# Performance work log

Measured on AMD Instinct MI355X. Metric: run time of the kernel, lower is better.

## Reference

```python
import jax, jax.numpy as jnp
import numpy as np

NUM_HEADS = 12
D_MODEL = 768
D_HEAD = D_MODEL // NUM_HEADS


def setup_inputs() -> dict:
    key = jax.random.key(0)
    k_x, k_wqkv, k_bqkv, k_wo, k_bo = jax.random.split(key, 5)
    B, S = 1, 4096
    x = jax.random.normal(k_x, (B, S, D_MODEL), dtype=jnp.float32)
    # flax Dense default init: lecun_normal for kernel, zeros for bias
    w_qkv = jax.random.normal(k_wqkv, (D_MODEL, 3 * D_MODEL), dtype=jnp.float32) / np.sqrt(D_MODEL)
    b_qkv = jnp.zeros((3 * D_MODEL,), dtype=jnp.float32)
    w_o = jax.random.normal(k_wo, (D_MODEL, D_MODEL), dtype=jnp.float32) / np.sqrt(D_MODEL)
    b_o = jnp.zeros((D_MODEL,), dtype=jnp.float32)
    return {"x": x, "w_qkv": w_qkv, "b_qkv": b_qkv, "w_o": w_o, "b_o": b_o}


def reference(x, w_qkv, b_qkv, w_o, b_o):
    B, S, _ = x.shape
    H, Dh = NUM_HEADS, D_HEAD
    qkv = jnp.einsum('bsd,de->bse', x, w_qkv) + b_qkv  # [B,S,3*D]
    q, k, v = jnp.split(qkv, 3, axis=-1)
    # [B,S,D] -> [B,H,S,Dh]
    q = q.reshape(B, S, H, Dh).transpose(0, 2, 1, 3)
    k = k.reshape(B, S, H, Dh).transpose(0, 2, 1, 3)
    v = v.reshape(B, S, H, Dh).transpose(0, 2, 1, 3)
    logits = jnp.einsum('bhqd,bhkd->bhqk', q, k) / jnp.sqrt(jnp.float32(Dh))
    weights = jax.nn.softmax(logits, axis=-1)  # deterministic=True -> no dropout
    attn = jnp.einsum('bhqk,bhkd->bhqd', weights, v)
    attn = attn.transpose(0, 2, 1, 3).reshape(B, S, H * Dh)
    return jnp.einsum('bsd,de->bse', attn, w_o) + b_o
```

## Files before the change

### kernel.cpp

```cpp
#include <hip/hip_runtime.h>

typedef unsigned short u16;
typedef __attribute__((ext_vector_type(8))) short bf16x8;
typedef __attribute__((ext_vector_type(4))) float f32x4;

#define CST 0.18033688011112042f

#if __has_builtin(__builtin_amdgcn_exp2f)
#define EXP2(x) __builtin_amdgcn_exp2f(x)
#else
#define EXP2(x) exp2f(x)
#endif

__device__ inline u16 f2bf(float f) {
    unsigned u;
    __builtin_memcpy(&u, &f, 4);
    unsigned r = (u + 0x7FFF + ((u >> 16) & 1)) >> 16;
    return (u16)r;
}
__device__ inline unsigned pack2(float lo, float hi) {
    return (unsigned)f2bf(lo) | ((unsigned)f2bf(hi) << 16);
}
__device__ inline unsigned fbits(float f) {
    unsigned u;
    __builtin_memcpy(&u, &f, 4);
    return u;
}
__device__ inline f32x4 fzero() {
    f32x4 z = {0.f, 0.f, 0.f, 0.f};
    return z;
}
__device__ inline f32x4 mfma16(bf16x8 a, bf16x8 b, f32x4 c) {
    return __builtin_amdgcn_mfma_f32_16x16x32_bf16(a, b, c, 0, 0, 0);
}

__device__ inline void gld_lds16(const u16* g, u16* l) {
    __builtin_amdgcn_global_load_lds(
        reinterpret_cast<const __attribute__((address_space(1))) unsigned int*>(
            reinterpret_cast<uintptr_t>(g)),
        reinterpret_cast<__attribute__((address_space(3))) unsigned int*>(
            static_cast<unsigned int>(reinterpret_cast<uintptr_t>(l))),
        16, 0, 0);
}

#define NB_WQKV (72 * 24)
#define NB_WO   (24 * 24)
#define NB_CVT  (4096 * 768 / 2048)

__global__ __launch_bounds__(256) void prep(const float* __restrict__ x,
                                            const float* __restrict__ w_qkv,
                                            const float* __restrict__ w_o,
                                            u16* __restrict__ xb,
                                            u16* __restrict__ wqkvT,
                                            u16* __restrict__ woT) {
    __shared__ float tile[32][33];
    int bid = blockIdx.x;
    int t = threadIdx.x;
    if (bid < NB_WQKV + NB_WO) {
        const float* in;
        u16* out;
        int bx, by, R, C;
        if (bid < NB_WQKV) {
            in = w_qkv; out = wqkvT; R = 768; C = 2304;
            bx = bid % 72; by = bid / 72;
        } else {
            int b2 = bid - NB_WQKV;
            in = w_o; out = woT; R = 768; C = 768;
            bx = b2 % 24; by = b2 / 24;
        }
        int c0 = bx * 32, r0 = by * 32;
        int tx = t & 31, ty = t >> 5;
#pragma unroll
        for (int j = 0; j < 32; j += 8)
            tile[ty + j][tx] = in[(size_t)(r0 + ty + j) * C + c0 + tx];
        __syncthreads();
#pragma unroll
        for (int j = 0; j < 32; j += 8)
            out[(size_t)(c0 + ty + j) * R + r0 + tx] = f2bf(tile[tx][ty + j]);
    } else {
        int i = (bid - NB_WQKV - NB_WO) * 2048 + t * 8;
        float4 a = *(const float4*)(x + i);
        float4 b = *(const float4*)(x + i + 4);
        uint4 w;
        w.x = pack2(a.x, a.y);
        w.y = pack2(a.z, a.w);
        w.z = pack2(b.x, b.y);
        w.w = pack2(b.z, b.w);
        *(uint4*)(xb + i) = w;
    }
}

__global__ __launch_bounds__(256) void vtrans(const u16* __restrict__ qkv,
                                              u16* __restrict__ vt) {
    __shared__ u16 T[64 * 136];
    int t = threadIdx.x;
    int h = blockIdx.y, kv0 = blockIdx.x * 128;
    {
        int key = t >> 1, ch = (t & 1) * 32;
        const u16* vp = qkv + (size_t)(kv0 + key) * 2304 + 1536 + h * 64 + ch;
        u16 tmp[32];
        *(uint4*)&tmp[0]  = *(const uint4*)vp;
        *(uint4*)&tmp[8]  = *(const uint4*)(vp + 8);
        *(uint4*)&tmp[16] = *(const uint4*)(vp + 16);
        *(uint4*)&tmp[24] = *(const uint4*)(vp + 24);
        int k5 = key & 31, grp = key >> 5;
        int kp = (grp << 5) | (((k5 >> 2) & 3) << 3) | ((k5 >> 4) << 2) | (k5 & 3);
#pragma unroll
        for (int j = 0; j < 32; j++) T[(ch + j) * 136 + kp] = tmp[j];
    }
    __syncthreads();
    {
        int dh = t >> 2, kc = (t & 3) * 32;
        uint4 o0 = *(const uint4*)&T[dh * 136 + kc];
        uint4 o1 = *(const uint4*)&T[dh * 136 + kc + 8];
        uint4 o2 = *(const uint4*)&T[dh * 136 + kc + 16];
        uint4 o3 = *(const uint4*)&T[dh * 136 + kc + 24];
        u16* op = vt + ((size_t)(h * 64 + dh)) * 4096 + kv0 + kc;
        *(uint4*)op = o0;
        *(uint4*)(op + 8) = o1;
        *(uint4*)(op + 16) = o2;
        *(uint4*)(op + 24) = o3;
    }
}

template <int MT, bool OUT_F32, bool SCALE_Q>
__global__ __launch_bounds__(256) void gemm_bt(const u16* __restrict__ A,
                                               const u16* __restrict__ Bt,
                                               const float* __restrict__ bias,
                                               void* __restrict__ Cv,
                                               int M, int N, int K) {
    constexpr int MI = MT / 32;
    constexpr int NA = MT / 64;
    constexpr int AH = MT * 32;
    constexpr int BH = 128 * 32;
    __shared__ u16 As[2 * AH];
    __shared__ u16 Bs[2 * BH];

    int t = threadIdx.x;
    int wave = t >> 6, lane = t & 63, quad = lane >> 4, l16 = lane & 15;

    int gx = gridDim.x;
    int flat = blockIdx.y * gx + blockIdx.x;
    int cpx = (gx * gridDim.y) >> 3;
    int swz = (flat & 7) * cpx + (flat >> 3);
    int bx = swz % gx, by = swz / gx;

    int mbase = by * MT, nbase = bx * 128;
    int mw = (wave & 1) * (MT / 2), nw = (wave >> 1) * 64;

    f32x4 acc[MI][4];
#pragma unroll
    for (int i = 0; i < MI; i++)
#pragma unroll
        for (int j = 0; j < 4; j++) acc[i][j] = fzero();

    int xqs = (lane & 3) ^ ((lane >> 3) & 3);
    const u16* AgL[NA];
    u16* AsL[NA];
#pragma unroll
    for (int j = 0; j < NA; j++) {
        int rl = wave * (MT / 4) + j * 16 + (lane >> 2);
        AgL[j] = A + (size_t)(mbase + rl) * K + xqs * 8;
        AsL[j] = As + wave * (MT / 4) * 32 + j * 512;
    }
    const u16* BgL[2];
    u16* BsL[2];
#pragma unroll
    for (int j = 0; j < 2; j++) {
        int rl = wave * 32 + j * 16 + (lane >> 2);
        BgL[j] = Bt + (size_t)(nbase + rl) * K + xqs * 8;
        BsL[j] = Bs + wave * 1024 + j * 512;
    }

    auto STAGE = [&](int buf, int kt) {
#pragma unroll
        for (int j = 0; j < NA; j++) gld_lds16(AgL[j] + kt, AsL[j] + buf * AH);
#pragma unroll
        for (int j = 0; j < 2; j++) gld_lds16(BgL[j] + kt, BsL[j] + buf * BH);
    };

    int xq = quad ^ ((l16 >> 1) & 3);
    int afo[MI], bfo[4];
#pragma unroll
    for (int i = 0; i < MI; i++) afo[i] = (mw + i * 16 + l16) * 32 + xq * 8;
#pragma unroll
    for (int i = 0; i < 4; i++) bfo[i] = (nw + i * 16 + l16) * 32 + xq * 8;

    STAGE(0, 0);
    __syncthreads();

    int cur = 0;
    for (int kt = 0; kt < K; kt += 32) {
        if (kt + 32 < K) STAGE(cur ^ 1, kt + 32);

        const u16* AsB = As + cur * AH;
        const u16* BsB = Bs + cur * BH;
        bf16x8 af[MI], bfr[4];
#pragma unroll
        for (int i = 0; i < MI; i++) af[i] = *(const bf16x8*)&AsB[afo[i]];
#pragma unroll
        for (int i = 0; i < 4; i++) bfr[i] = *(const bf16x8*)&BsB[bfo[i]];
#pragma unroll
        for (int mi = 0; mi < MI; mi++)
#pragma unroll
            for (int ni = 0; ni < 4; ni++)
                acc[mi][ni] = mfma16(af[mi], bfr[ni], acc[mi][ni]);

        __syncthreads();
        cur ^= 1;
    }

#pragma unroll
    for (int ni = 0; ni < 4; ni++) {
        int col = nbase + nw + ni * 16 + l16;
        float bv = bias[col];
        float scale = (SCALE_Q && col < 768) ? CST : 1.0f;
#pragma unroll
        for (int mi = 0; mi < MI; mi++) {
#pragma unroll
            for (int r = 0; r < 4; r++) {
                int row = mbase + mw + mi * 16 + quad * 4 + r;
                float v = (acc[mi][ni][r] + bv) * scale;
                if (OUT_F32)
                    ((float*)Cv)[(size_t)row * N + col] = v;
                else
                    ((u16*)Cv)[(size_t)row * N + col] = f2bf(v);
            }
        }
    }
}

#define SEQ 4096
#define QKV_LD 2304

__global__ __launch_bounds__(256, 4) void attn_flash(const u16* __restrict__ qkv,
                                                     const u16* __restrict__ vt,
                                                     u16* __restrict__ attn) {
    __shared__ __align__(16) char smem[32768];

    int t = threadIdx.x;
    int wave = t >> 6, lane = t & 63, quad = lane >> 4, l16 = lane & 15;
    int kw = wave & 1, qw = wave >> 1;

    int flat = blockIdx.y * 64 + blockIdx.x;
    int swz = (flat & 7) * 96 + (flat >> 3);
    int h = swz >> 6;
    int q0 = (swz & 63) * 64;
    const int QOFF = h * 64, KOFF = 768 + h * 64;

    bf16x8 qf[2][2];
#pragma unroll
    for (int qs = 0; qs < 2; qs++) {
        const u16* qp = qkv + (size_t)(q0 + qw * 32 + qs * 16 + l16) * QKV_LD + QOFF + quad * 8;
        qf[qs][0] = *(const bf16x8*)(qp);
        qf[qs][1] = *(const bf16x8*)(qp + 32);
    }

    f32x4 o[2][4];
    f32x4 lacc[2];
#pragma unroll
    for (int qs = 0; qs < 2; qs++) {
        lacc[qs] = fzero();
#pragma unroll
        for (int j = 0; j < 4; j++) o[qs][j] = fzero();
    }
    bf16x8 vones;
#pragma unroll
    for (int j = 0; j < 8; j++) vones[j] = (short)0x3F80;

    const u16* kgl[2];
    const u16* vgl[2];
    int sofs[2];
#pragma unroll
    for (int j = 0; j < 2; j++) {
        int r = wave * 16 + j * 8 + (lane >> 3);
        int cd = (lane & 7) ^ ((lane >> 3) & 7);
        kgl[j] = qkv + (size_t)r * QKV_LD + KOFF + cd * 8;
        vgl[j] = vt + (size_t)(h * 64 + r) * SEQ + cd * 8;
        sofs[j] = (wave * 16 + j * 8) * 64;
    }

    auto STAGE = [&](int buf, int kv) {
        u16* kb = (u16*)(smem + buf * 8192);
        u16* vb = (u16*)(smem + 16384 + buf * 8192);
#pragma unroll
        for (int j = 0; j < 2; j++) gld_lds16(kgl[j] + (size_t)kv * QKV_LD, kb + sofs[j]);
#pragma unroll
        for (int j = 0; j < 2; j++) gld_lds16(vgl[j] + kv, vb + sofs[j]);
    };

    STAGE(0, 0);
    __syncthreads();

    int cur = 0;
    int x7 = l16 & 7;
    for (int kv0 = 0; kv0 < SEQ; kv0 += 64) {
        if (kv0 + 64 < SEQ) STAGE(cur ^ 1, kv0 + 64);

        const u16* KsB = (const u16*)(smem + cur * 8192);
        const u16* VsB = (const u16*)(smem + 16384 + cur * 8192);

        bf16x8 kf[2][2];
#pragma unroll
        for (int st = 0; st < 2; st++) {
            int r = kw * 32 + st * 16 + l16;
            kf[st][0] = *(const bf16x8*)&KsB[r * 64 + (quad ^ x7) * 8];
            kf[st][1] = *(const bf16x8*)&KsB[r * 64 + ((quad + 4) ^ x7) * 8];
        }
        bf16x8 vf[4];
#pragma unroll
        for (int nt = 0; nt < 4; nt++) {
            int r = nt * 16 + l16;
            vf[nt] = *(const bf16x8*)&VsB[r * 64 + ((kw * 4 + quad) ^ x7) * 8];
        }

        __builtin_amdgcn_s_setprio(1);
#pragma unroll
        for (int qs = 0; qs < 2; qs++) {
            f32x4 s0 = mfma16(kf[0][0], qf[qs][0], fzero());
            s0 = mfma16(kf[0][1], qf[qs][1], s0);
            f32x4 s1 = mfma16(kf[1][0], qf[qs][0], fzero());
            s1 = mfma16(kf[1][1], qf[qs][1], s1);
            float p00 = EXP2(s0[0]), p01 = EXP2(s0[1]);
            float p02 = EXP2(s0[2]), p03 = EXP2(s0[3]);
            float p10 = EXP2(s1[0]), p11 = EXP2(s1[1]);
            float p12 = EXP2(s1[2]), p13 = EXP2(s1[3]);
            uint4 pk;
            pk.x = __builtin_amdgcn_perm(fbits(p01), fbits(p00), 0x07060302u);
            pk.y = __builtin_amdgcn_perm(fbits(p03), fbits(p02), 0x07060302u);
            pk.z = __builtin_amdgcn_perm(fbits(p11), fbits(p10), 0x07060302u);
            pk.w = __builtin_amdgcn_perm(fbits(p13), fbits(p12), 0x07060302u);
            bf16x8 pf;
            __builtin_memcpy(&pf, &pk, 16);
            lacc[qs] = mfma16(pf, vones, lacc[qs]);
#pragma unroll
            for (int nt = 0; nt < 4; nt++)
                o[qs][nt] = mfma16(pf, vf[nt], o[qs][nt]);
        }
        __builtin_amdgcn_s_setprio(0);

        __syncthreads();
        cur ^= 1;
    }

    float* M0 = (float*)smem;
    float* Lm = (float*)(smem + 17408);
    if (l16 == 0) {
#pragma unroll
        for (int qs = 0; qs < 2; qs++)
#pragma unroll
            for (int r = 0; r < 4; r++)
                Lm[kw * 64 + qw * 32 + qs * 16 + quad * 4 + r] = lacc[qs][r];
    }
    if (kw == 1) {
#pragma unroll
        for (int nt = 0; nt < 4; nt++)
#pragma unroll
            for (int r = 0; r < 4; r++)
                M0[(qw * 32 + quad * 4 + r) * 68 + nt * 16 + l16] = o[0][nt][r];
    } else {
#pragma unroll
        for (int nt = 0; nt < 4; nt++)
#pragma unroll
            for (int r = 0; r < 4; r++)
                M0[(qw * 32 + 16 + quad * 4 + r) * 68 + nt * 16 + l16] = o[1][nt][r];
    }
    __syncthreads();
    if (kw == 0) {
#pragma unroll
        for (int r = 0; r < 4; r++) {
            int rw = qw * 32 + quad * 4 + r;
            float ltot = Lm[rw] + Lm[64 + rw];
            float inv = 1.0f / ltot;
            u16* op = attn + (size_t)(q0 + rw) * 768 + h * 64;
#pragma unroll
            for (int nt = 0; nt < 4; nt++) {
                float v = o[0][nt][r] + M0[rw * 68 + nt * 16 + l16];
                op[nt * 16 + l16] = f2bf(v * inv);
            }
        }
    } else {
#pragma unroll
        for (int r = 0; r < 4; r++) {
            int rw = qw * 32 + 16 + quad * 4 + r;
            float ltot = Lm[rw] + Lm[64 + rw];
            float inv = 1.0f / ltot;
            u16* op = attn + (size_t)(q0 + rw) * 768 + h * 64;
#pragma unroll
            for (int nt = 0; nt < 4; nt++) {
                float v = o[1][nt][r] + M0[rw * 68 + nt * 16 + l16];
                op[nt * 16 + l16] = f2bf(v * inv);
            }
        }
    }
}

extern "C" void kernel_launch(void* const* d_in, const int* in_sizes, int n_in,
                              void* d_out, int out_size, void* d_ws, size_t ws_size,
                              hipStream_t stream) {
    const float* x      = (const float*)d_in[0];
    const float* w_qkv  = (const float*)d_in[1];
    const float* b_qkv  = (const float*)d_in[2];
    const float* w_o    = (const float*)d_in[3];
    const float* b_o    = (const float*)d_in[4];
    float* out = (float*)d_out;

    u16* wqkvT = (u16*)d_ws;
    u16* woT   = wqkvT + (size_t)2304 * 768;
    u16* qkv   = woT + (size_t)768 * 768;
    u16* attnb = qkv + (size_t)4096 * 2304;
    u16* Vt    = attnb + (size_t)4096 * 768;
    u16* xb    = attnb;

    prep<<<dim3(NB_WQKV + NB_WO + NB_CVT), 256, 0, stream>>>(
        x, w_qkv, w_o, xb, wqkvT, woT);

    gemm_bt<128, false, true><<<dim3(2304 / 128, 4096 / 128), 256, 0, stream>>>(
        xb, wqkvT, b_qkv, qkv, 4096, 2304, 768);

    vtrans<<<dim3(SEQ / 128, 12), 256, 0, stream>>>(qkv, Vt);

    attn_flash<<<dim3(SEQ / 64, 12), 256, 0, stream>>>(qkv, Vt, attnb);

    gemm_bt<64, true, false><<<dim3(768 / 128, 4096 / 64), 256, 0, stream>>>(
        attnb, woT, b_o, out, 4096, 768, 768);
}
```

Measured before the change: 177.7 us.

## Fuse V transpose into QKV GEMM epilogue and shrink output-projection N tile

Removes the separate vtrans kernel. The QKV GEMM blocks that cover the V columns now write their bias-added tile transposed through shared memory straight into the Vt buffer, in the permuted key order attention expects. The V block of qkv is no longer written and read back. The GEMM template also gains an NT parameter, and the output projection now uses 64x64 tiles, doubling its grid to give more blocks for occupancy. The cost is extra syncs and an LDS staging pass in the V blocks, plus smaller tiles in the last GEMM, which lowers per-block data reuse.

```diff
diff --git a/kernel.cpp b/kernel.cpp
--- a/kernel.cpp
+++ b/kernel.cpp
@@ -5,6 +5,8 @@
 typedef __attribute__((ext_vector_type(4))) float f32x4;
 
 #define CST 0.18033688011112042f
+#define SEQ 4096
+#define QKV_LD 2304
 
 #if __has_builtin(__builtin_amdgcn_exp2f)
 #define EXP2(x) __builtin_amdgcn_exp2f(x)
@@ -90,51 +92,22 @@
     }
 }
 
-__global__ __launch_bounds__(256) void vtrans(const u16* __restrict__ qkv,
-                                              u16* __restrict__ vt) {
-    __shared__ u16 T[64 * 136];
-    int t = threadIdx.x;
-    int h = blockIdx.y, kv0 = blockIdx.x * 128;
-    {
-        int key = t >> 1, ch = (t & 1) * 32;
-        const u16* vp = qkv + (size_t)(kv0 + key) * 2304 + 1536 + h * 64 + ch;
-        u16 tmp[32];
-        *(uint4*)&tmp[0]  = *(const uint4*)vp;
-        *(uint4*)&tmp[8]  = *(const uint4*)(vp + 8);
-        *(uint4*)&tmp[16] = *(const uint4*)(vp + 16);
-        *(uint4*)&tmp[24] = *(const uint4*)(vp + 24);
-        int k5 = key & 31, grp = key >> 5;
-        int kp = (grp << 5) | (((k5 >> 2) & 3) << 3) | ((k5 >> 4) << 2) | (k5 & 3);
-#pragma unroll
-        for (int j = 0; j < 32; j++) T[(ch + j) * 136 + kp] = tmp[j];
-    }
-    __syncthreads();
-    {
-        int dh = t >> 2, kc = (t & 3) * 32;
-        uint4 o0 = *(const uint4*)&T[dh * 136 + kc];
-        uint4 o1 = *(const uint4*)&T[dh * 136 + kc + 8];
-        uint4 o2 = *(const uint4*)&T[dh * 136 + kc + 16];
-        uint4 o3 = *(const uint4*)&T[dh * 136 + kc + 24];
-        u16* op = vt + ((size_t)(h * 64 + dh)) * 4096 + kv0 + kc;
-        *(uint4*)op = o0;
-        *(uint4*)(op + 8) = o1;
-        *(uint4*)(op + 16) = o2;
-        *(uint4*)(op + 24) = o3;
-    }
-}
-
-template <int MT, bool OUT_F32, bool SCALE_Q>
+template <int MT, int NT, bool OUT_F32, bool SCALE_Q, bool FUSE_VT>
 __global__ __launch_bounds__(256) void gemm_bt(const u16* __restrict__ A,
                                                const u16* __restrict__ Bt,
                                                const float* __restrict__ bias,
                                                void* __restrict__ Cv,
+                                               u16* __restrict__ vt,
                                                int M, int N, int K) {
     constexpr int MI = MT / 32;
+    constexpr int NI = NT / 32;
     constexpr int NA = MT / 64;
+    constexpr int NB = NT / 64;
     constexpr int AH = MT * 32;
-    constexpr int BH = 128 * 32;
-    __shared__ u16 As[2 * AH];
-    __shared__ u16 Bs[2 * BH];
+    constexpr int BH = NT * 32;
+    __shared__ u16 pool[2 * AH + 2 * BH];
+    u16* As = pool;
+    u16* Bs = pool + 2 * AH;
 
     int t = threadIdx.x;
     int wave = t >> 6, lane = t & 63, quad = lane >> 4, l16 = lane & 15;
@@ -145,14 +118,14 @@
     int swz = (flat & 7) * cpx + (flat >> 3);
     int bx = swz % gx, by = swz / gx;
 
-    int mbase = by * MT, nbase = bx * 128;
-    int mw = (wave & 1) * (MT / 2), nw = (wave >> 1) * 64;
-
-    f32x4 acc[MI][4];
+    int mbase = by * MT, nbase = bx * NT;
+    int mw = (wave & 1) * (MT / 2), nw = (wave >> 1) * (NT / 2);
+
+    f32x4 acc[MI][NI];
 #pragma unroll
     for (int i = 0; i < MI; i++)
 #pragma unroll
-        for (int j = 0; j < 4; j++) acc[i][j] = fzero();
+        for (int j = 0; j < NI; j++) acc[i][j] = fzero();
 
     int xqs = (lane & 3) ^ ((lane >> 3) & 3);
     const u16* AgL[NA];
@@ -163,28 +136,28 @@
         AgL[j] = A + (size_t)(mbase + rl) * K + xqs * 8;
         AsL[j] = As + wave * (MT / 4) * 32 + j * 512;
     }
-    const u16* BgL[2];
-    u16* BsL[2];
-#pragma unroll
-    for (int j = 0; j < 2; j++) {
-        int rl = wave * 32 + j * 16 + (lane >> 2);
+    const u16* BgL[NB];
+    u16* BsL[NB];
+#pragma unroll
+    for (int j = 0; j < NB; j++) {
+        int rl = wave * (NT / 4) + j * 16 + (lane >> 2);
         BgL[j] = Bt + (size_t)(nbase + rl) * K + xqs * 8;
-        BsL[j] = Bs + wave * 1024 + j * 512;
+        BsL[j] = Bs + wave * (NT / 4) * 32 + j * 512;
     }
 
     auto STAGE = [&](int buf, int kt) {
 #pragma unroll
         for (int j = 0; j < NA; j++) gld_lds16(AgL[j] + kt, AsL[j] + buf * AH);
 #pragma unroll
-        for (int j = 0; j < 2; j++) gld_lds16(BgL[j] + kt, BsL[j] + buf * BH);
+        for (int j = 0; j < NB; j++) gld_lds16(BgL[j] + kt, BsL[j] + buf * BH);
     };
 
     int xq = quad ^ ((l16 >> 1) & 3);
-    int afo[MI], bfo[4];
+    int afo[MI], bfo[NI];
 #pragma unroll
     for (int i = 0; i < MI; i++) afo[i] = (mw + i * 16 + l16) * 32 + xq * 8;
 #pragma unroll
-    for (int i = 0; i < 4; i++) bfo[i] = (nw + i * 16 + l16) * 32 + xq * 8;
+    for (int i = 0; i < NI; i++) bfo[i] = (nw + i * 16 + l16) * 32 + xq * 8;
 
     STAGE(0, 0);
     __syncthreads();
@@ -195,23 +168,65 @@
 
         const u16* AsB = As + cur * AH;
         const u16* BsB = Bs + cur * BH;
-        bf16x8 af[MI], bfr[4];
+        bf16x8 af[MI], bfr[NI];
 #pragma unroll
         for (int i = 0; i < MI; i++) af[i] = *(const bf16x8*)&AsB[afo[i]];
 #pragma unroll
-        for (int i = 0; i < 4; i++) bfr[i] = *(const bf16x8*)&BsB[bfo[i]];
+        for (int i = 0; i < NI; i++) bfr[i] = *(const bf16x8*)&BsB[bfo[i]];
 #pragma unroll
         for (int mi = 0; mi < MI; mi++)
 #pragma unroll
-            for (int ni = 0; ni < 4; ni++)
+            for (int ni = 0; ni < NI; ni++)
                 acc[mi][ni] = mfma16(af[mi], bfr[ni], acc[mi][ni]);
 
         __syncthreads();
         cur ^= 1;
     }
 
-#pragma unroll
-    for (int ni = 0; ni < 4; ni++) {
+    if (FUSE_VT && nbase >= 1536) {
+        u16* T = pool;
+        int h0 = (nbase - 1536) >> 6;
+#pragma unroll
+        for (int pp = 0; pp < 2; pp++) {
+            if ((wave & 1) == pp) {
+#pragma unroll
+                for (int ni = 0; ni < NI; ni++) {
+                    int col = nw + ni * 16 + l16;
+                    float bv = bias[nbase + col];
+#pragma unroll
+                    for (int mi = 0; mi < MI; mi++) {
+#pragma unroll
+                        for (int r = 0; r < 4; r++) {
+                            int rowl = mi * 16 + quad * 4 + r;
+                            int k5 = rowl & 31, grp = rowl >> 5;
+                            int kp = (grp << 5) | (((k5 >> 2) & 3) << 3) |
+                                     ((k5 >> 4) << 2) | (k5 & 3);
+                            T[col * 72 + kp] = f2bf(acc[mi][ni][r] + bv);
+                        }
+                    }
+                }
+            }
+            __syncthreads();
+            {
+                int dh = t >> 1, kc = (t & 1) * 32;
+                const u16* src = &T[dh * 72 + kc];
+                uint4 o0 = *(const uint4*)(src);
+                uint4 o1 = *(const uint4*)(src + 8);
+                uint4 o2 = *(const uint4*)(src + 16);
+                uint4 o3 = *(const uint4*)(src + 24);
+                u16* op = vt + (size_t)(h0 * 64 + dh) * SEQ + mbase + pp * 64 + kc;
+                *(uint4*)op = o0;
+                *(uint4*)(op + 8) = o1;
+                *(uint4*)(op + 16) = o2;
+                *(uint4*)(op + 24) = o3;
+            }
+            __syncthreads();
+        }
+        return;
+    }
+
+#pragma unroll
+    for (int ni = 0; ni < NI; ni++) {
         int col = nbase + nw + ni * 16 + l16;
         float bv = bias[col];
         float scale = (SCALE_Q && col < 768) ? CST : 1.0f;
@@ -229,9 +244,6 @@
         }
     }
 }
-
-#define SEQ 4096
-#define QKV_LD 2304
 
 __global__ __launch_bounds__(256, 4) void attn_flash(const u16* __restrict__ qkv,
                                                      const u16* __restrict__ vt,
@@ -415,13 +427,13 @@
     prep<<<dim3(NB_WQKV + NB_WO + NB_CVT), 256, 0, stream>>>(
         x, w_qkv, w_o, xb, wqkvT, woT);
 
-    gemm_bt<128, false, true><<<dim3(2304 / 128, 4096 / 128), 256, 0, stream>>>(
-        xb, wqkvT, b_qkv, qkv, 4096, 2304, 768);
-
-    vtrans<<<dim3(SEQ / 128, 12), 256, 0, stream>>>(qkv, Vt);
+    gemm_bt<128, 128, false, true, true>
+        <<<dim3(2304 / 128, 4096 / 128), 256, 0, stream>>>(
+            xb, wqkvT, b_qkv, qkv, Vt, 4096, 2304, 768);
 
     attn_flash<<<dim3(SEQ / 64, 12), 256, 0, stream>>>(qkv, Vt, attnb);
 
-    gemm_bt<64, true, false><<<dim3(768 / 128, 4096 / 64), 256, 0, stream>>>(
-        attnb, woT, b_o, out, 4096, 768, 768);
-}
+    gemm_bt<64, 64, true, false, false>
+        <<<dim3(768 / 64, 4096 / 64), 256, 0, stream>>>(
+            attnb, woT, b_o, out, nullptr, 4096, 768, 768);
+}
```

Measured after the change: 183.9 us. +3.5%, slower.
